# Optimization experiments

Hardware: AMD Instinct MI355X
Metric: run time of the kernel (lower is better)

Reference implementation:

```python
import jax, jax.numpy as jnp
import numpy as np

NUM_CLASSES = 80
AFS = 1024          # actors_features_size
OFS = 2048          # objects_features_size
NHEADS = 4
NHID = AFS // NHEADS + 4 // NHEADS   # 257
D = AFS + 4                           # 1028
ALPHA = 0.2                           # LeakyReLU slope
N_ACT, N_OBJ = 512, 3584


def _gat(x, adj_mask, W, a):
    # x: [N, D]; W: [H, D, NHID]; a: [H, 2*NHID]; adj_mask: [N, N] bool
    Wh = jnp.einsum('nf,hfd->hnd', x, W)                      # [H, N, NHID]
    f1 = jnp.einsum('hnd,hd->hn', Wh, a[:, :NHID])            # src score
    f2 = jnp.einsum('hnd,hd->hn', Wh, a[:, NHID:])            # dst score
    e = f1[:, :, None] + f2[:, None, :]                       # [H, N, N]
    e = jnp.where(e > 0, e, ALPHA * e)                        # LeakyReLU
    e = jnp.where(adj_mask[None], e, jnp.asarray(-9e15, e.dtype))
    att = jax.nn.softmax(e, axis=-1)                          # [H, N, N]
    h = jnp.einsum('hnm,hmd->hnd', att, Wh)                   # [H, N, NHID]
    h = jax.nn.elu(h)
    return jnp.transpose(h, (1, 0, 2)).reshape(x.shape[0], NHEADS * NHID)


def _ln(x, g, b):
    m = jnp.mean(x, axis=-1, keepdims=True)
    v = jnp.mean((x - m) ** 2, axis=-1, keepdims=True)
    return (x - m) * jax.lax.rsqrt(v + 1e-5) * g + b


def setup_inputs() -> dict:
    key = jax.random.key(0)
    ks = jax.random.split(key, 24)
    d = {
        'actors_features': jax.random.normal(ks[0], (N_ACT, 1024, 4, 7, 7), jnp.float32),
        'actors_labels': jax.random.uniform(ks[1], (N_ACT, NUM_CLASSES), jnp.float32),
        'actors_boxes': jax.random.uniform(ks[2], (N_ACT, 4), jnp.float32),
        'objects_features': jax.random.normal(ks[3], (N_OBJ, OFS), jnp.float32),
        'objects_boxes': jax.random.uniform(ks[4], (N_OBJ, 4), jnp.float32),
        'adj': jax.random.randint(ks[5], (N_ACT + N_OBJ, N_ACT + N_OBJ), 0, 2, jnp.int32),
    }
    s = lambda k, shp, fan: jax.random.normal(k, shp, jnp.float32) * (1.0 / np.sqrt(fan))
    d['obj_W'] = s(ks[6], (OFS, AFS), OFS)
    d['obj_b'] = jnp.zeros((AFS,), jnp.float32)
    d['gat1_W'] = s(ks[7], (NHEADS, D, NHID), D)
    d['gat1_a'] = s(ks[8], (NHEADS, 2 * NHID), 2 * NHID)
    d['gat_fc_W'] = s(ks[9], (D, D), D)
    d['gat_fc_b'] = jnp.zeros((D,), jnp.float32)
    d['ln1_g'] = jnp.ones((D,), jnp.float32)
    d['ln1_b'] = jnp.zeros((D,), jnp.float32)
    d['gat2_W'] = s(ks[10], (NHEADS, D, NHID), D)
    d['gat2_a'] = s(ks[11], (NHEADS, 2 * NHID), 2 * NHID)
    d['gat_fc2_W'] = s(ks[12], (D, D), D)
    d['gat_fc2_b'] = jnp.zeros((D,), jnp.float32)
    d['ln2_g'] = jnp.ones((D,), jnp.float32)
    d['ln2_b'] = jnp.zeros((D,), jnp.float32)
    d['logits_W'] = s(ks[13], (D, NUM_CLASSES), D)
    d['logits_b'] = jnp.zeros((NUM_CLASSES,), jnp.float32)
    return d


def reference(actors_features, actors_labels, actors_boxes, objects_features,
              objects_boxes, adj, obj_W, obj_b, gat1_W, gat1_a, gat_fc_W,
              gat_fc_b, ln1_g, ln1_b, gat2_W, gat2_a, gat_fc2_W, gat_fc2_b,
              ln2_g, ln2_b, logits_W, logits_b):
    ab, ob = actors_boxes, objects_boxes
    a_geo = jnp.stack([ab[:, 3] - ab[:, 1], ab[:, 2] - ab[:, 0],
                       (ab[:, 2] - ab[:, 0]) / 2 + ab[:, 0],
                       (ab[:, 3] - ab[:, 1]) / 2 + ab[:, 1]], axis=1)
    o_geo = jnp.stack([ob[:, 3] - ob[:, 1], ob[:, 2] - ob[:, 0],
                       (ob[:, 2] - ob[:, 0]) / 2 + ob[:, 0],
                       (ob[:, 3] - ob[:, 1]) / 2 + ob[:, 1]], axis=1)
    # torch.no_grad mean-pool over T,H,W -> [N, C]
    af = jax.lax.stop_gradient(jnp.mean(actors_features, axis=(2, 3, 4)))
    af = jnp.concatenate([af, a_geo], axis=1)                 # [Na, D]
    of = jax.nn.relu(objects_features @ obj_W + obj_b)        # reducer (OFS>AFS)
    of = jnp.concatenate([of, o_geo], axis=1)                 # [No, D]
    x = jnp.concatenate([af, of], axis=0)                     # [N, D]
    mask = adj > 0
    g = _gat(x, mask, gat1_W, gat1_a)
    x = _ln(x + g @ gat_fc_W + gat_fc_b, ln1_g, ln1_b)
    g = _gat(x, mask, gat2_W, gat2_a)
    x = _ln(x + g @ gat_fc2_W + gat_fc2_b, ln2_g, ln2_b)
    logits = x[:af.shape[0]] @ logits_W + logits_b            # [Na, C]
    y = actors_labels
    loss = jnp.mean(jnp.clip(logits, 0, None) - logits * y
                    + jnp.log1p(jnp.exp(-jnp.abs(logits))))
    return jax.nn.sigmoid(logits), loss
```

## Files before the change

kernel.cpp:

```cpp
#include <hip/hip_runtime.h>
#include <cstdint>

#define NACT 512
#define NOBJ 3584
#define NTOT 4096
#define DCOLS 1028
#define NHID_ 257
#define OFSZ 2048
#define KPAD 1056
#define NPADH 320
#define NWH   1280
#define NPADFC 1152

typedef float f32x4 __attribute__((ext_vector_type(4)));
typedef short short8v __attribute__((ext_vector_type(8)));
typedef short short4v __attribute__((ext_vector_type(4)));

static const size_t OFF_X0    = 0;
static const size_t OFF_T     = 4210688;
static const size_t OFF_F1    = 8421376;
static const size_t OFF_F2    = 8437760;
static const size_t OFF_RMAX  = 8454144;
static const size_t OFF_RDEN  = 8470528;
static const size_t OFF_LOSSP = 8486912;
static const size_t OFF_MASK  = 8487424;
static const size_t OFF_XB    = 9011712;
static const size_t OFF_GB    = 11174400;
static const size_t OFF_OFB   = 13337088;
static const size_t OFF_OBJWT = 17007104;
static const size_t OFF_GATWT = 18055680;
static const size_t OFF_FCWT  = 19407360;
static const size_t OFF_WHT   = 20623872;

__device__ __forceinline__ short f2bf(float x) {
    unsigned u = __float_as_uint(x);
    u += 0x7fffu + ((u >> 16) & 1u);
    return (short)(u >> 16);
}
__device__ __forceinline__ int swz(int row, int chunk) {
    return row * 64 + (((chunk ^ ((row >> 1) & 3))) << 4);
}
__device__ __forceinline__ void gload16(const void* g, void* l) {
    __builtin_amdgcn_global_load_lds(
        (const __attribute__((address_space(1))) unsigned int*)g,
        (__attribute__((address_space(3))) unsigned int*)l, 16, 0, 0);
}

__global__ void k_geo(const float* __restrict__ ab, const float* __restrict__ ob,
                      float* __restrict__ X, short* __restrict__ Xb) {
    int n = blockIdx.x * blockDim.x + threadIdx.x;
    if (n >= NTOT) return;
    const float* b = (n < NACT) ? &ab[n * 4] : &ob[(n - NACT) * 4];
    float x0 = b[0], y0 = b[1], x1 = b[2], y1 = b[3];
    float g0 = y1 - y0, g1 = x1 - x0;
    float g2 = (x1 - x0) * 0.5f + x0, g3 = (y1 - y0) * 0.5f + y0;
    float* o = &X[(size_t)n * DCOLS + 1024];
    o[0] = g0; o[1] = g1; o[2] = g2; o[3] = g3;
    short* ob2 = &Xb[(size_t)n * KPAD + 1024];
    ob2[0] = f2bf(g0); ob2[1] = f2bf(g1); ob2[2] = f2bf(g2); ob2[3] = f2bf(g3);
}

__global__ __launch_bounds__(256) void k_meanpool(const float* __restrict__ af,
                                                  float* __restrict__ X,
                                                  short* __restrict__ Xb) {
    int w = blockIdx.x * 4 + (threadIdx.x >> 6);
    int lane = threadIdx.x & 63;
    const float* src = af + (size_t)w * 196;
    float s = src[lane] + src[lane + 64] + src[lane + 128];
    if (lane < 4) s += src[192 + lane];
    #pragma unroll
    for (int off = 32; off; off >>= 1) s += __shfl_down(s, off);
    if (lane == 0) {
        int n = w >> 10, c = w & 1023;
        float v = s * (1.0f / 196.0f);
        X[(size_t)n * DCOLS + c] = v;
        Xb[(size_t)n * KPAD + c] = f2bf(v);
    }
}

__global__ __launch_bounds__(256) void k_packmask(const int* __restrict__ adj,
                                                  unsigned long long* __restrict__ mb) {
    int w = blockIdx.x * 4 + (threadIdx.x >> 6);
    int lane = threadIdx.x & 63;
    int v = adj[(size_t)w * 64 + lane];
    unsigned long long m = __ballot(v > 0);
    if (lane == 0) mb[w] = m;
}

__global__ __launch_bounds__(256) void k_convF(const float* __restrict__ src,
                                               short* __restrict__ dst, int n8) {
    int i = blockIdx.x * 256 + threadIdx.x;
    if (i >= n8) return;
    float4 a = *reinterpret_cast<const float4*>(src + (size_t)i * 8);
    float4 b = *reinterpret_cast<const float4*>(src + (size_t)i * 8 + 4);
    short8v o;
    o[0]=f2bf(a.x); o[1]=f2bf(a.y); o[2]=f2bf(a.z); o[3]=f2bf(a.w);
    o[4]=f2bf(b.x); o[5]=f2bf(b.y); o[6]=f2bf(b.z); o[7]=f2bf(b.w);
    *reinterpret_cast<short8v*>(dst + (size_t)i * 8) = o;
}

__global__ __launch_bounds__(256) void k_transpW(const float* __restrict__ W, int K, int N,
                                                 short* __restrict__ Wt, int Kpad) {
    __shared__ float Ws[32][33];
    int k0 = blockIdx.x * 32, n0 = blockIdx.y * 32;
    int t = threadIdx.x;
    #pragma unroll
    for (int i = 0; i < 4; ++i) {
        int j = t + i * 256;
        int r = j >> 5, c = j & 31;
        float v = 0.f;
        if (k0 + r < K && n0 + c < N) v = W[(size_t)(k0 + r) * N + n0 + c];
        Ws[r][c] = v;
    }
    __syncthreads();
    #pragma unroll
    for (int i = 0; i < 4; ++i) {
        int j = t + i * 256;
        int n = j >> 5, k = j & 31;
        Wt[(size_t)(n0 + n) * Kpad + k0 + k] = f2bf(Ws[k][n]);
    }
}

template <int MODE>
__global__ __launch_bounds__(256, 2) void k_mm(
    const short* __restrict__ Ab, int lda,
    const short* __restrict__ Bt, int ldb,
    void* __restrict__ Cptr, int ldc,
    const float* __restrict__ bias,
    const float* __restrict__ resid, int ldr,
    float* __restrict__ F1, float* __restrict__ F2,
    const float* __restrict__ AV,
    short* __restrict__ Cbf,
    int nk, int Nvalid) {
    __shared__ char sm[32768];
    const int t = threadIdx.x;
    const int m0 = blockIdx.x * 128;
    const int n0 = blockIdx.y * 128;
    const int wv = t >> 6, lane = t & 63, lr = lane & 15, lk = lane >> 4;
    const int wr = wv >> 1, wc = wv & 1;

    int aoff[4], boff[4];
    #pragma unroll
    for (int i = 0; i < 4; ++i) aoff[i] = swz(64 * wr + 16 * i + lr, lk);
    #pragma unroll
    for (int j = 0; j < 4; ++j) boff[j] = 8192 + swz(64 * wc + 16 * j + lr, lk);

    f32x4 acc[4][4];
    #pragma unroll
    for (int i = 0; i < 4; ++i)
        #pragma unroll
        for (int j = 0; j < 4; ++j) acc[i][j] = (f32x4){0.f, 0.f, 0.f, 0.f};

    auto stage = [&](int p, int k0) {
        char* base = sm + p * 16384;
        #pragma unroll
        for (int c = 0; c < 2; ++c) {
            int slot = 2 * wv + c;
            int row = slot * 16 + (lane >> 2);
            int gch = (lane & 3) ^ ((row >> 1) & 3);
            gload16(Ab + (size_t)(m0 + row) * lda + k0 + gch * 8, base + slot * 1024);
            gload16(Bt + (size_t)(n0 + row) * ldb + k0 + gch * 8, base + 8192 + slot * 1024);
        }
    };

    stage(0, 0);
    __syncthreads();
    int p = 0;
    for (int kt = 0; kt < nk; ++kt) {
        if (kt + 1 < nk) stage(p ^ 1, (kt + 1) * 32);
        const char* cb = sm + p * 16384;
        short8v a[4], b[4];
        #pragma unroll
        for (int i = 0; i < 4; ++i) a[i] = *reinterpret_cast<const short8v*>(cb + aoff[i]);
        #pragma unroll
        for (int j = 0; j < 4; ++j) b[j] = *reinterpret_cast<const short8v*>(cb + boff[j]);
        #pragma unroll
        for (int i = 0; i < 4; ++i)
            #pragma unroll
            for (int j = 0; j < 4; ++j)
                acc[i][j] = __builtin_amdgcn_mfma_f32_16x16x32_bf16(a[i], b[j], acc[i][j], 0, 0, 0);
        __syncthreads();
        p ^= 1;
    }

    const int mb0 = m0 + 64 * wr + 4 * lk;
    if constexpr (MODE == 0 || MODE == 3) {
        float* Cf = (float*)Cptr;
        #pragma unroll
        for (int i = 0; i < 4; ++i)
            #pragma unroll
            for (int j = 0; j < 4; ++j) {
                int c = n0 + 64 * wc + 16 * j + lr;
                if (c < Nvalid) {
                    #pragma unroll
                    for (int rr = 0; rr < 4; ++rr) {
                        int m = mb0 + 16 * i + rr;
                        float v = acc[i][j][rr] + bias[c];
                        if constexpr (MODE == 0) v = fmaxf(v, 0.0f);
                        if constexpr (MODE == 3) v += resid[(size_t)m * ldr + c];
                        Cf[(size_t)m * ldc + c] = v;
                        if constexpr (MODE == 0) Cbf[(size_t)m * KPAD + c] = f2bf(v);
                    }
                }
            }
    } else {
        const int cwbase = n0 + 64 * wc;
        const int h = cwbase / NPADH;
        const int dwbase = cwbase - h * NPADH;
        const float* AVh = AV + h * (2 * NHID_);
        float* F1h = F1 + h * NTOT;
        float* F2h = F2 + h * NTOT;
        short* CwhH = (short*)Cptr + (size_t)h * ((size_t)NPADH * NTOT);
        float la1[4], la2[4];
        #pragma unroll
        for (int j = 0; j < 4; ++j) {
            int d = dwbase + 16 * j + lr;
            la1[j] = (d < NHID_) ? AVh[d] : 0.f;
            la2[j] = (d < NHID_) ? AVh[NHID_ + d] : 0.f;
        }
        #pragma unroll
        for (int i = 0; i < 4; ++i) {
            #pragma unroll
            for (int j = 0; j < 4; ++j) {
                int d = dwbase + 16 * j + lr;
                short4v o;
                o[0] = f2bf(acc[i][j][0]); o[1] = f2bf(acc[i][j][1]);
                o[2] = f2bf(acc[i][j][2]); o[3] = f2bf(acc[i][j][3]);
                *reinterpret_cast<short4v*>(&CwhH[(size_t)d * NTOT + mb0 + 16 * i]) = o;
            }
            #pragma unroll
            for (int rr = 0; rr < 4; ++rr) {
                float s1 = 0.f, s2 = 0.f;
                #pragma unroll
                for (int j = 0; j < 4; ++j) {
                    s1 += acc[i][j][rr] * la1[j];
                    s2 += acc[i][j][rr] * la2[j];
                }
                #pragma unroll
                for (int mk = 1; mk < 16; mk <<= 1) {
                    s1 += __shfl_xor(s1, mk);
                    s2 += __shfl_xor(s2, mk);
                }
                if (lr == 0) {
                    int m = mb0 + 16 * i + rr;
                    atomicAdd(&F1h[m], s1);
                    atomicAdd(&F2h[m], s2);
                }
            }
        }
    }
}

__global__ __launch_bounds__(256, 2) void k_pv(
    const short* __restrict__ WHT,
    const float* __restrict__ F1, const float* __restrict__ F2,
    const float* __restrict__ RMAX, const float* __restrict__ RDEN,
    const unsigned long long* __restrict__ MB,
    short* __restrict__ Gb) {
    __shared__ char sm[49152];
    const int t = threadIdx.x;
    const int i0 = blockIdx.x;
    const int xcd = i0 & 7, slot = i0 >> 3;
    const int h = xcd >> 1;
    const int m0 = (slot * 2 + (xcd & 1)) * 64;
    const short* WhH = WHT + (size_t)h * ((size_t)NPADH * NTOT);
    const float* F2h = F2 + h * NTOT;
    const int gcol = h * NHID_;

    const int pr = t >> 2, pq = t & 3;
    const int n = m0 + pr;
    const float f1n = F1[h * NTOT + n];
    const float rmx = RMAX[h * NTOT + n];
    const float psc = 1.0f / RDEN[h * NTOT + n];
    const unsigned long long* mrow = MB + (size_t)n * 64;

    const int wv = t >> 6, lane = t & 63, lr = lane & 15, lk = lane >> 4;
    int aoff[4], boff[5];
    #pragma unroll
    for (int i = 0; i < 4; ++i) aoff[i] = swz(16 * i + lr, lk);
    #pragma unroll
    for (int j = 0; j < 5; ++j) boff[j] = 4096 + swz(80 * wv + 16 * j + lr, lk);

    f32x4 acc[4][5];
    #pragma unroll
    for (int i = 0; i < 4; ++i)
        #pragma unroll
        for (int j = 0; j < 5; ++j) acc[i][j] = (f32x4){0.f, 0.f, 0.f, 0.f};

    auto stageV = [&](int p, int k0) {
        char* vb = sm + p * 24576 + 4096;
        #pragma unroll
        for (int c = 0; c < 5; ++c) {
            int slot2 = 5 * wv + c;
            int row = slot2 * 16 + (lane >> 2);
            int gch = (lane & 3) ^ ((row >> 1) & 3);
            gload16(WhH + (size_t)row * NTOT + k0 + gch * 8, vb + slot2 * 1024);
        }
    };
    auto pgen = [&](int p, int k0) {
        const int mk = k0 + pq * 8;
        unsigned long long wbits = mrow[k0 >> 6] >> ((k0 & 63) + pq * 8);
        float4 q0 = *reinterpret_cast<const float4*>(F2h + mk);
        float4 q1 = *reinterpret_cast<const float4*>(F2h + mk + 4);
        float fv[8] = {q0.x, q0.y, q0.z, q0.w, q1.x, q1.y, q1.z, q1.w};
        short8v o;
        #pragma unroll
        for (int j = 0; j < 8; ++j) {
            float e = f1n + fv[j];
            e = e > 0.f ? e : 0.2f * e;
            float pvv = ((wbits >> j) & 1ULL) ? __expf(e - rmx) * psc : 0.f;
            o[j] = f2bf(pvv);
        }
        *reinterpret_cast<short8v*>(sm + p * 24576 + swz(pr, pq)) = o;
    };

    stageV(0, 0);
    pgen(0, 0);
    __syncthreads();
    int p = 0;
    for (int kt = 0; kt < NTOT / 32; ++kt) {
        if (kt + 1 < NTOT / 32) {
            stageV(p ^ 1, (kt + 1) * 32);
            pgen(p ^ 1, (kt + 1) * 32);
        }
        const char* cb = sm + p * 24576;
        short8v a[4], b[5];
        #pragma unroll
        for (int i = 0; i < 4; ++i) a[i] = *reinterpret_cast<const short8v*>(cb + aoff[i]);
        #pragma unroll
        for (int j = 0; j < 5; ++j) b[j] = *reinterpret_cast<const short8v*>(cb + boff[j]);
        #pragma unroll
        for (int i = 0; i < 4; ++i)
            #pragma unroll
            for (int j = 0; j < 5; ++j)
                acc[i][j] = __builtin_amdgcn_mfma_f32_16x16x32_bf16(a[i], b[j], acc[i][j], 0, 0, 0);
        __syncthreads();
        p ^= 1;
    }

    #pragma unroll
    for (int j = 0; j < 5; ++j) {
        int d = 80 * wv + 16 * j + lr;
        if (d < NHID_) {
            #pragma unroll
            for (int i = 0; i < 4; ++i)
                #pragma unroll
                for (int rr = 0; rr < 4; ++rr) {
                    int m = m0 + 16 * i + 4 * lk + rr;
                    float v = acc[i][j][rr];
                    v = v > 0.f ? v : expm1f(v);
                    Gb[(size_t)m * KPAD + gcol + d] = f2bf(v);
                }
        }
    }
}

__global__ __launch_bounds__(256) void k_rowstat(const float* __restrict__ F1,
                                                 const float* __restrict__ F2,
                                                 const unsigned long long* __restrict__ mb,
                                                 float* __restrict__ RMAX, float* __restrict__ RDEN) {
    __shared__ float f2s[NTOT];
    __shared__ unsigned long long mw[4][64];
    int h = blockIdx.y;
    const float4* src = reinterpret_cast<const float4*>(F2 + (size_t)h * NTOT);
    float4* dst = reinterpret_cast<float4*>(f2s);
    for (int i = threadIdx.x; i < NTOT / 4; i += 256) dst[i] = src[i];
    int wv = threadIdx.x >> 6, lane = threadIdx.x & 63;
    int n = blockIdx.x * 4 + wv;
    mw[wv][lane] = mb[(size_t)n * 64 + lane];
    __syncthreads();
    float f1n = F1[(size_t)h * NTOT + n];
    float rm = -1e30f, rs = 0.f;
    for (int b = 0; b < 64; ++b) {
        unsigned long long wb = mw[wv][b];
        if ((wb >> lane) & 1ULL) {
            float e = f1n + f2s[b * 64 + lane];
            e = e > 0.f ? e : 0.2f * e;
            if (e > rm) { rs *= __expf(rm - e); rm = e; }
            rs += __expf(e - rm);
        }
    }
    #pragma unroll
    for (int off = 32; off; off >>= 1) {
        float m2 = __shfl_down(rm, off), s2 = __shfl_down(rs, off);
        float nm = fmaxf(rm, m2);
        rs = rs * __expf(rm - nm) + s2 * __expf(m2 - nm);
        rm = nm;
    }
    if (lane == 0) {
        if (rs == 0.f) rs = 1.f;
        RMAX[(size_t)h * NTOT + n] = rm;
        RDEN[(size_t)h * NTOT + n] = rs;
    }
}

__global__ __launch_bounds__(256) void k_ln(const float* __restrict__ T,
                                            const float* __restrict__ g,
                                            const float* __restrict__ b,
                                            float* __restrict__ O,
                                            short* __restrict__ xb) {
    int n = blockIdx.x;
    const float* row = T + (size_t)n * DCOLS;
    float s = 0.f, q = 0.f;
    for (int i = threadIdx.x; i < DCOLS / 4; i += 256) {
        float4 v = *reinterpret_cast<const float4*>(&row[i * 4]);
        s += v.x + v.y + v.z + v.w;
        q += v.x * v.x + v.y * v.y + v.z * v.z + v.w * v.w;
    }
    __shared__ float ls[2][4];
    int lane = threadIdx.x & 63, wv = threadIdx.x >> 6;
    #pragma unroll
    for (int off = 32; off; off >>= 1) {
        s += __shfl_down(s, off);
        q += __shfl_down(q, off);
    }
    if (lane == 0) { ls[0][wv] = s; ls[1][wv] = q; }
    __syncthreads();
    s = ls[0][0] + ls[0][1] + ls[0][2] + ls[0][3];
    q = ls[1][0] + ls[1][1] + ls[1][2] + ls[1][3];
    float mean = s * (1.0f / DCOLS);
    float var = q * (1.0f / DCOLS) - mean * mean;
    float rstd = rsqrtf(var + 1e-5f);
    float* orow = O + (size_t)n * DCOLS;
    for (int i = threadIdx.x; i < DCOLS; i += 256) {
        float v = (row[i] - mean) * rstd * g[i] + b[i];
        orow[i] = v;
        if (xb) xb[(size_t)n * KPAD + i] = f2bf(v);
    }
}

__global__ __launch_bounds__(128) void k_logits(const float* __restrict__ X,
                                                const float* __restrict__ W,
                                                const float* __restrict__ bias,
                                                const float* __restrict__ Y,
                                                float* __restrict__ out,
                                                float* __restrict__ lossp) {
    __shared__ float xs[DCOLS];
    int n = blockIdx.x;
    for (int i = threadIdx.x; i < DCOLS / 4; i += 128)
        *reinterpret_cast<float4*>(&xs[i * 4]) =
            *reinterpret_cast<const float4*>(&X[(size_t)n * DCOLS + i * 4]);
    __syncthreads();
    float loss = 0.f;
    int c = threadIdx.x;
    if (c < 80) {
        float acc = bias[c];
        for (int k = 0; k < DCOLS; ++k) acc += xs[k] * W[k * 80 + c];
        out[n * 80 + c] = 1.0f / (1.0f + expf(-acc));
        float y = Y[n * 80 + c];
        loss = fmaxf(acc, 0.f) - acc * y + log1pf(expf(-fabsf(acc)));
    }
    __shared__ float lr[2];
    int lane = threadIdx.x & 63, wv = threadIdx.x >> 6;
    #pragma unroll
    for (int off = 32; off; off >>= 1) loss += __shfl_down(loss, off);
    if (lane == 0) lr[wv] = loss;
    __syncthreads();
    if (threadIdx.x == 0) lossp[n] = lr[0] + lr[1];
}

__global__ __launch_bounds__(256) void k_lossfin(const float* __restrict__ lossp,
                                                 float* __restrict__ out) {
    float s = 0.f;
    for (int i = threadIdx.x; i < NACT; i += 256) s += lossp[i];
    #pragma unroll
    for (int off = 32; off; off >>= 1) s += __shfl_down(s, off);
    __shared__ float lr[4];
    int lane = threadIdx.x & 63, wv = threadIdx.x >> 6;
    if (lane == 0) lr[wv] = s;
    __syncthreads();
    if (threadIdx.x == 0) out[NACT * 80] = (lr[0] + lr[1] + lr[2] + lr[3]) / (float)(NACT * 80);
}

extern "C" void kernel_launch(void* const* d_in, const int* in_sizes, int n_in,
                              void* d_out, int out_size, void* d_ws, size_t ws_size,
                              hipStream_t stream) {
    const float* actors_features  = (const float*)d_in[0];
    const float* actors_labels    = (const float*)d_in[1];
    const float* actors_boxes     = (const float*)d_in[2];
    const float* objects_features = (const float*)d_in[3];
    const float* objects_boxes    = (const float*)d_in[4];
    const int*   adj              = (const int*)d_in[5];
    const float* obj_W    = (const float*)d_in[6];
    const float* obj_b    = (const float*)d_in[7];
    const float* gatW[2]  = {(const float*)d_in[8],  (const float*)d_in[14]};
    const float* gatA[2]  = {(const float*)d_in[9],  (const float*)d_in[15]};
    const float* fcW[2]   = {(const float*)d_in[10], (const float*)d_in[16]};
    const float* fcB[2]   = {(const float*)d_in[11], (const float*)d_in[17]};
    const float* lnG[2]   = {(const float*)d_in[12], (const float*)d_in[18]};
    const float* lnB[2]   = {(const float*)d_in[13], (const float*)d_in[19]};
    const float* logits_W = (const float*)d_in[20];
    const float* logits_b = (const float*)d_in[21];
    float* out = (float*)d_out;

    float* ws   = (float*)d_ws;
    float* X0   = ws + OFF_X0;
    float* T    = ws + OFF_T;
    float* F1   = ws + OFF_F1;
    float* F2   = ws + OFF_F2;
    float* RMAX = ws + OFF_RMAX;
    float* RDEN = ws + OFF_RDEN;
    float* LOSSP= ws + OFF_LOSSP;
    unsigned long long* MASK = (unsigned long long*)(ws + OFF_MASK);
    short* Xb    = (short*)(ws + OFF_XB);
    short* Gb    = (short*)(ws + OFF_GB);
    short* OFb   = (short*)(ws + OFF_OFB);
    short* objWt = (short*)(ws + OFF_OBJWT);
    short* gatWt = (short*)(ws + OFF_GATWT);
    short* fcWt  = (short*)(ws + OFF_FCWT);
    short* WHT   = (short*)(ws + OFF_WHT);

    hipMemsetAsync(F1, 0, 2 * 4 * NTOT * sizeof(float), stream);
    hipMemsetAsync(Gb, 0, (size_t)NTOT * KPAD * 2, stream);
    hipMemsetAsync(Xb, 0, (size_t)NTOT * KPAD * 2, stream);

    k_geo<<<(NTOT + 255) / 256, 256, 0, stream>>>(actors_boxes, objects_boxes, X0, Xb);
    k_meanpool<<<(NACT * 1024) / 4, 256, 0, stream>>>(actors_features, X0, Xb);
    k_packmask<<<(NTOT * 64) / 4, 256, 0, stream>>>(adj, MASK);
    k_convF<<<(NOBJ * OFSZ / 8 + 255) / 256, 256, 0, stream>>>(objects_features, OFb, NOBJ * OFSZ / 8);

    k_transpW<<<dim3(64, 32), 256, 0, stream>>>(obj_W, OFSZ, 1024, objWt, OFSZ);
    for (int L = 0; L < 2; ++L) {
        for (int h = 0; h < 4; ++h)
            k_transpW<<<dim3(33, 10), 256, 0, stream>>>(
                gatW[L] + (size_t)h * DCOLS * NHID_, DCOLS, NHID_,
                gatWt + (size_t)L * NWH * KPAD + (size_t)h * NPADH * KPAD, KPAD);
        k_transpW<<<dim3(33, 36), 256, 0, stream>>>(
            fcW[L], DCOLS, DCOLS, fcWt + (size_t)L * NPADFC * KPAD, KPAD);
    }

    k_mm<0><<<dim3(NOBJ / 128, 1024 / 128), 256, 0, stream>>>(
        OFb, OFSZ, objWt, OFSZ, X0 + (size_t)NACT * DCOLS, DCOLS,
        obj_b, nullptr, 0, nullptr, nullptr, nullptr,
        Xb + (size_t)NACT * KPAD, OFSZ / 32, 1024);

    const float* xin = X0;
    for (int L = 0; L < 2; ++L) {
        if (L == 1)
            hipMemsetAsync(F1, 0, 2 * 4 * NTOT * sizeof(float), stream);
        k_mm<1><<<dim3(NTOT / 128, NWH / 128), 256, 0, stream>>>(
            Xb, KPAD, gatWt + (size_t)L * NWH * KPAD, KPAD, WHT, 0,
            nullptr, nullptr, 0, F1, F2, gatA[L], nullptr,
            KPAD / 32, NHID_);
        k_rowstat<<<dim3(NTOT / 4, 4), 256, 0, stream>>>(F1, F2, MASK, RMAX, RDEN);
        k_pv<<<256, 256, 0, stream>>>(WHT, F1, F2, RMAX, RDEN, MASK, Gb);
        k_mm<3><<<dim3(NTOT / 128, NPADFC / 128), 256, 0, stream>>>(
            Gb, KPAD, fcWt + (size_t)L * NPADFC * KPAD, KPAD, T, DCOLS,
            fcB[L], xin, DCOLS, nullptr, nullptr, nullptr, nullptr,
            KPAD / 32, DCOLS);
        k_ln<<<NTOT, 256, 0, stream>>>(T, lnG[L], lnB[L], T, (L == 0) ? Xb : nullptr);
        xin = T;
    }
    k_logits<<<NACT, 128, 0, stream>>>(T, logits_W, logits_b, actors_labels, out, LOSSP);
    k_lossfin<<<1, 256, 0, stream>>>(LOSSP, out);
}
```

Before: 1.432 ms.

## Halve GEMM and attention-PV tile sizes to double block count, add MFMA priority

The shared GEMM body now uses 128x64 tiles, with each wave owning 32 rows, and runs under launch bounds allowing 3 blocks per CU. The PV kernel now processes 32 query rows per block and launches 512 blocks, with P generation using 4-wide chunks and a new swizzle. s_setprio is raised around the MFMA loops in both kernels. The goal is more blocks, and so more occupancy and better CU fill on a 256-CU part, at the cost of less operand reuse per block and more global and LDS traffic per FLOP.

Measured after the change: 1.396 ms. 2.5% less time.

```diff
diff --git a/kernel.cpp b/kernel.cpp
--- a/kernel.cpp
+++ b/kernel.cpp
@@ -122,7 +122,7 @@
 }
 
 template <int MODE>
-__global__ __launch_bounds__(256, 2) void k_mm(
+__device__ __forceinline__ void mm_body(
     const short* __restrict__ Ab, int lda,
     const short* __restrict__ Bt, int ldb,
     void* __restrict__ Cptr, int ldc,
@@ -132,34 +132,37 @@
     const float* __restrict__ AV,
     short* __restrict__ Cbf,
     int nk, int Nvalid) {
-    __shared__ char sm[32768];
+    __shared__ char sm[24576];
     const int t = threadIdx.x;
     const int m0 = blockIdx.x * 128;
-    const int n0 = blockIdx.y * 128;
+    const int n0 = blockIdx.y * 64;
     const int wv = t >> 6, lane = t & 63, lr = lane & 15, lk = lane >> 4;
-    const int wr = wv >> 1, wc = wv & 1;
-
-    int aoff[4], boff[4];
-    #pragma unroll
-    for (int i = 0; i < 4; ++i) aoff[i] = swz(64 * wr + 16 * i + lr, lk);
-    #pragma unroll
-    for (int j = 0; j < 4; ++j) boff[j] = 8192 + swz(64 * wc + 16 * j + lr, lk);
-
-    f32x4 acc[4][4];
-    #pragma unroll
-    for (int i = 0; i < 4; ++i)
+
+    int aoff[2], boff[4];
+    #pragma unroll
+    for (int i = 0; i < 2; ++i) aoff[i] = swz(32 * wv + 16 * i + lr, lk);
+    #pragma unroll
+    for (int j = 0; j < 4; ++j) boff[j] = 8192 + swz(16 * j + lr, lk);
+
+    f32x4 acc[2][4];
+    #pragma unroll
+    for (int i = 0; i < 2; ++i)
         #pragma unroll
         for (int j = 0; j < 4; ++j) acc[i][j] = (f32x4){0.f, 0.f, 0.f, 0.f};
 
     auto stage = [&](int p, int k0) {
-        char* base = sm + p * 16384;
+        char* base = sm + p * 12288;
         #pragma unroll
         for (int c = 0; c < 2; ++c) {
             int slot = 2 * wv + c;
             int row = slot * 16 + (lane >> 2);
             int gch = (lane & 3) ^ ((row >> 1) & 3);
             gload16(Ab + (size_t)(m0 + row) * lda + k0 + gch * 8, base + slot * 1024);
-            gload16(Bt + (size_t)(n0 + row) * ldb + k0 + gch * 8, base + 8192 + slot * 1024);
+        }
+        {
+            int row = wv * 16 + (lane >> 2);
+            int gch = (lane & 3) ^ ((row >> 1) & 3);
+            gload16(Bt + (size_t)(n0 + row) * ldb + k0 + gch * 8, base + 8192 + wv * 1024);
         }
     };
 
@@ -168,29 +171,31 @@
     int p = 0;
     for (int kt = 0; kt < nk; ++kt) {
         if (kt + 1 < nk) stage(p ^ 1, (kt + 1) * 32);
-        const char* cb = sm + p * 16384;
-        short8v a[4], b[4];
-        #pragma unroll
-        for (int i = 0; i < 4; ++i) a[i] = *reinterpret_cast<const short8v*>(cb + aoff[i]);
+        const char* cb = sm + p * 12288;
+        short8v a[2], b[4];
+        #pragma unroll
+        for (int i = 0; i < 2; ++i) a[i] = *reinterpret_cast<const short8v*>(cb + aoff[i]);
         #pragma unroll
         for (int j = 0; j < 4; ++j) b[j] = *reinterpret_cast<const short8v*>(cb + boff[j]);
-        #pragma unroll
-        for (int i = 0; i < 4; ++i)
+        __builtin_amdgcn_s_setprio(1);
+        #pragma unroll
+        for (int i = 0; i < 2; ++i)
             #pragma unroll
             for (int j = 0; j < 4; ++j)
                 acc[i][j] = __builtin_amdgcn_mfma_f32_16x16x32_bf16(a[i], b[j], acc[i][j], 0, 0, 0);
+        __builtin_amdgcn_s_setprio(0);
         __syncthreads();
         p ^= 1;
     }
 
-    const int mb0 = m0 + 64 * wr + 4 * lk;
+    const int mb0 = m0 + 32 * wv + 4 * lk;
     if constexpr (MODE == 0 || MODE == 3) {
         float* Cf = (float*)Cptr;
         #pragma unroll
-        for (int i = 0; i < 4; ++i)
+        for (int i = 0; i < 2; ++i)
             #pragma unroll
             for (int j = 0; j < 4; ++j) {
-                int c = n0 + 64 * wc + 16 * j + lr;
+                int c = n0 + 16 * j + lr;
                 if (c < Nvalid) {
                     #pragma unroll
                     for (int rr = 0; rr < 4; ++rr) {
@@ -204,9 +209,8 @@
                 }
             }
     } else {
-        const int cwbase = n0 + 64 * wc;
-        const int h = cwbase / NPADH;
-        const int dwbase = cwbase - h * NPADH;
+        const int h = n0 / NPADH;
+        const int dwbase = n0 - h * NPADH;
         const float* AVh = AV + h * (2 * NHID_);
         float* F1h = F1 + h * NTOT;
         float* F2h = F2 + h * NTOT;
@@ -219,7 +223,7 @@
             la2[j] = (d < NHID_) ? AVh[NHID_ + d] : 0.f;
         }
         #pragma unroll
-        for (int i = 0; i < 4; ++i) {
+        for (int i = 0; i < 2; ++i) {
             #pragma unroll
             for (int j = 0; j < 4; ++j) {
                 int d = dwbase + 16 * j + lr;
@@ -251,23 +255,40 @@
     }
 }
 
+__global__ __launch_bounds__(256, 3) void k_mm_obj(
+    const short* Ab, int lda, const short* Bt, int ldb, void* C, int ldc,
+    const float* bias, short* Cbf, int nk, int Nvalid) {
+    mm_body<0>(Ab, lda, Bt, ldb, C, ldc, bias, nullptr, 0, nullptr, nullptr, nullptr, Cbf, nk, Nvalid);
+}
+__global__ __launch_bounds__(256, 3) void k_mm_wh(
+    const short* Ab, int lda, const short* Bt, int ldb, void* C,
+    float* F1, float* F2, const float* AV, int nk) {
+    mm_body<1>(Ab, lda, Bt, ldb, C, 0, nullptr, nullptr, 0, F1, F2, AV, nullptr, nk, NHID_);
+}
+__global__ __launch_bounds__(256, 3) void k_mm_fc(
+    const short* Ab, int lda, const short* Bt, int ldb, void* C, int ldc,
+    const float* bias, const float* resid, int ldr, int nk, int Nvalid) {
+    mm_body<3>(Ab, lda, Bt, ldb, C, ldc, bias, resid, ldr, nullptr, nullptr, nullptr, nullptr, nk, Nvalid);
+}
+
 __global__ __launch_bounds__(256, 2) void k_pv(
     const short* __restrict__ WHT,
     const float* __restrict__ F1, const float* __restrict__ F2,
     const float* __restrict__ RMAX, const float* __restrict__ RDEN,
     const unsigned long long* __restrict__ MB,
     short* __restrict__ Gb) {
-    __shared__ char sm[49152];
+    __shared__ char sm[45056];
     const int t = threadIdx.x;
     const int i0 = blockIdx.x;
-    const int xcd = i0 & 7, slot = i0 >> 3;
+    const int xcd = i0 & 7, kk = i0 >> 3;
     const int h = xcd >> 1;
-    const int m0 = (slot * 2 + (xcd & 1)) * 64;
+    const int s = (kk << 1) | (xcd & 1);
+    const int m0 = s * 32;
     const short* WhH = WHT + (size_t)h * ((size_t)NPADH * NTOT);
     const float* F2h = F2 + h * NTOT;
     const int gcol = h * NHID_;
 
-    const int pr = t >> 2, pq = t & 3;
+    const int pr = t >> 3, pq = t & 7;
     const int n = m0 + pr;
     const float f1n = F1[h * NTOT + n];
     const float rmx = RMAX[h * NTOT + n];
@@ -275,20 +296,20 @@
     const unsigned long long* mrow = MB + (size_t)n * 64;
 
     const int wv = t >> 6, lane = t & 63, lr = lane & 15, lk = lane >> 4;
-    int aoff[4], boff[5];
-    #pragma unroll
-    for (int i = 0; i < 4; ++i) aoff[i] = swz(16 * i + lr, lk);
-    #pragma unroll
-    for (int j = 0; j < 5; ++j) boff[j] = 4096 + swz(80 * wv + 16 * j + lr, lk);
-
-    f32x4 acc[4][5];
-    #pragma unroll
-    for (int i = 0; i < 4; ++i)
+    int aoff[2], boff[5];
+    #pragma unroll
+    for (int i = 0; i < 2; ++i) aoff[i] = swz(16 * i + lr, lk);
+    #pragma unroll
+    for (int j = 0; j < 5; ++j) boff[j] = 2048 + swz(80 * wv + 16 * j + lr, lk);
+
+    f32x4 acc[2][5];
+    #pragma unroll
+    for (int i = 0; i < 2; ++i)
         #pragma unroll
         for (int j = 0; j < 5; ++j) acc[i][j] = (f32x4){0.f, 0.f, 0.f, 0.f};
 
     auto stageV = [&](int p, int k0) {
-        char* vb = sm + p * 24576 + 4096;
+        char* vb = sm + p * 22528 + 2048;
         #pragma unroll
         for (int c = 0; c < 5; ++c) {
             int slot2 = 5 * wv + c;
@@ -298,20 +319,20 @@
         }
     };
     auto pgen = [&](int p, int k0) {
-        const int mk = k0 + pq * 8;
-        unsigned long long wbits = mrow[k0 >> 6] >> ((k0 & 63) + pq * 8);
+        const int mk = k0 + pq * 4;
+        unsigned long long wbits = mrow[k0 >> 6] >> ((k0 & 63) + pq * 4);
         float4 q0 = *reinterpret_cast<const float4*>(F2h + mk);
-        float4 q1 = *reinterpret_cast<const float4*>(F2h + mk + 4);
-        float fv[8] = {q0.x, q0.y, q0.z, q0.w, q1.x, q1.y, q1.z, q1.w};
-        short8v o;
-        #pragma unroll
-        for (int j = 0; j < 8; ++j) {
+        float fv[4] = {q0.x, q0.y, q0.z, q0.w};
+        short4v o;
+        #pragma unroll
+        for (int j = 0; j < 4; ++j) {
             float e = f1n + fv[j];
             e = e > 0.f ? e : 0.2f * e;
             float pvv = ((wbits >> j) & 1ULL) ? __expf(e - rmx) * psc : 0.f;
             o[j] = f2bf(pvv);
         }
-        *reinterpret_cast<short8v*>(sm + p * 24576 + swz(pr, pq)) = o;
+        int off = pr * 64 + ((((pq >> 1) ^ ((pr >> 1) & 3)) << 4) + (pq & 1) * 8);
+        *reinterpret_cast<short4v*>(sm + p * 22528 + off) = o;
     };
 
     stageV(0, 0);
@@ -323,17 +344,19 @@
             stageV(p ^ 1, (kt + 1) * 32);
             pgen(p ^ 1, (kt + 1) * 32);
         }
-        const char* cb = sm + p * 24576;
-        short8v a[4], b[5];
-        #pragma unroll
-        for (int i = 0; i < 4; ++i) a[i] = *reinterpret_cast<const short8v*>(cb + aoff[i]);
+        const char* cb = sm + p * 22528;
+        short8v a[2], b[5];
+        #pragma unroll
+        for (int i = 0; i < 2; ++i) a[i] = *reinterpret_cast<const short8v*>(cb + aoff[i]);
         #pragma unroll
         for (int j = 0; j < 5; ++j) b[j] = *reinterpret_cast<const short8v*>(cb + boff[j]);
-        #pragma unroll
-        for (int i = 0; i < 4; ++i)
+        __builtin_amdgcn_s_setprio(1);
+        #pragma unroll
+        for (int i = 0; i < 2; ++i)
             #pragma unroll
             for (int j = 0; j < 5; ++j)
                 acc[i][j] = __builtin_amdgcn_mfma_f32_16x16x32_bf16(a[i], b[j], acc[i][j], 0, 0, 0);
+        __builtin_amdgcn_s_setprio(0);
         __syncthreads();
         p ^= 1;
     }
@@ -343,7 +366,7 @@
         int d = 80 * wv + 16 * j + lr;
         if (d < NHID_) {
             #pragma unroll
-            for (int i = 0; i < 4; ++i)
+            for (int i = 0; i < 2; ++i)
                 #pragma unroll
                 for (int rr = 0; rr < 4; ++rr) {
                     int m = m0 + 16 * i + 4 * lk + rr;
@@ -529,25 +552,21 @@
             fcW[L], DCOLS, DCOLS, fcWt + (size_t)L * NPADFC * KPAD, KPAD);
     }
 
-    k_mm<0><<<dim3(NOBJ / 128, 1024 / 128), 256, 0, stream>>>(
+    k_mm_obj<<<dim3(NOBJ / 128, 1024 / 64), 256, 0, stream>>>(
         OFb, OFSZ, objWt, OFSZ, X0 + (size_t)NACT * DCOLS, DCOLS,
-        obj_b, nullptr, 0, nullptr, nullptr, nullptr,
-        Xb + (size_t)NACT * KPAD, OFSZ / 32, 1024);
+        obj_b, Xb + (size_t)NACT * KPAD, OFSZ / 32, 1024);
 
     const float* xin = X0;
     for (int L = 0; L < 2; ++L) {
         if (L == 1)
             hipMemsetAsync(F1, 0, 2 * 4 * NTOT * sizeof(float), stream);
-        k_mm<1><<<dim3(NTOT / 128, NWH / 128), 256, 0, stream>>>(
-            Xb, KPAD, gatWt + (size_t)L * NWH * KPAD, KPAD, WHT, 0,
-            nullptr, nullptr, 0, F1, F2, gatA[L], nullptr,
-            KPAD / 32, NHID_);
+        k_mm_wh<<<dim3(NTOT / 128, NWH / 64), 256, 0, stream>>>(
+            Xb, KPAD, gatWt + (size_t)L * NWH * KPAD, KPAD, WHT, F1, F2, gatA[L], KPAD / 32);
         k_rowstat<<<dim3(NTOT / 4, 4), 256, 0, stream>>>(F1, F2, MASK, RMAX, RDEN);
-        k_pv<<<256, 256, 0, stream>>>(WHT, F1, F2, RMAX, RDEN, MASK, Gb);
-        k_mm<3><<<dim3(NTOT / 128, NPADFC / 128), 256, 0, stream>>>(
+        k_pv<<<512, 256, 0, stream>>>(WHT, F1, F2, RMAX, RDEN, MASK, Gb);
+        k_mm_fc<<<dim3(NTOT / 128, NPADFC / 64), 256, 0, stream>>>(
             Gb, KPAD, fcWt + (size_t)L * NPADFC * KPAD, KPAD, T, DCOLS,
-            fcB[L], xin, DCOLS, nullptr, nullptr, nullptr, nullptr,
-            KPAD / 32, DCOLS);
+            fcB[L], xin, DCOLS, KPAD / 32, DCOLS);
         k_ln<<<NTOT, 256, 0, stream>>>(T, lnG[L], lnB[L], T, (L == 0) ? Xb : nullptr);
         xin = T;
     }
```
